# Performance work log

Measured on AMD Instinct MI355X. Metric: run time of the kernel, lower is better.

The kernel has to match this reference:

```python
import jax, jax.numpy as jnp
import numpy as np


def _graph_conv(feat_src, e_src, e_dst, n_src, n_dst, W, b):
    # DGL GraphConv, norm='both', bipartite block; feat_src: [N_src, A, C, H]
    ones_e = jnp.ones(e_src.shape[0], dtype=feat_src.dtype)
    out_deg = jax.ops.segment_sum(ones_e, e_src, num_segments=n_src)
    in_deg = jax.ops.segment_sum(ones_e, e_dst, num_segments=n_dst)
    norm_src = jnp.clip(out_deg, 1.0) ** -0.5
    norm_dst = jnp.clip(in_deg, 1.0) ** -0.5
    feat = feat_src * norm_src[:, None, None, None]
    # in_feats == out_feats -> DGL multiplies by W before aggregation
    feat = jnp.einsum('nach,ho->naco', feat, W)
    msgs = feat[e_src]                                   # gather  [E, A, C, H]
    agg = jax.ops.segment_sum(msgs, e_dst, num_segments=n_dst)  # scatter-add
    return agg * norm_dst[:, None, None, None] + b


def setup_inputs() -> dict:
    key = jax.random.key(0)
    ks = jax.random.split(key, 8)
    H = 128
    N_SRC0, N_DST0, N_DST1 = 50000, 20000, 4096
    E0, E1 = 320000, 65536
    return {
        'in_feat': jax.random.normal(ks[0], (2, H, 2, N_SRC0), dtype=jnp.float32),
        'W': jax.random.normal(ks[1], (H, H), dtype=jnp.float32) / np.sqrt(H),
        'b': jnp.zeros((H,), dtype=jnp.float32),
        'e0_src': jax.random.randint(ks[2], (E0,), 0, N_SRC0, dtype=jnp.int32),
        'e0_dst': jax.random.randint(ks[3], (E0,), 0, N_DST0, dtype=jnp.int32),
        'e1_src': jax.random.randint(ks[4], (E1,), 0, N_DST0, dtype=jnp.int32),
        'e1_dst': jax.random.randint(ks[5], (E1,), 0, N_DST1, dtype=jnp.int32),
        'n_dst0': N_DST0,
        'n_dst1': N_DST1,
    }


def reference(in_feat, W, b, e0_src, e0_dst, e1_src, e1_dst, n_dst0, n_dst1):
    # [A, H, C, N] -> [N, A, C, H]
    x = jnp.transpose(in_feat, (3, 0, 2, 1))
    n_src0 = x.shape[0]
    h = _graph_conv(x, e0_src, e0_dst, n_src0, n_dst0, W, b)
    h = jax.nn.relu(h)
    h = _graph_conv(h, e1_src, e1_dst, n_dst0, n_dst1, W, b)
    h = jax.nn.relu(h)
    # [N_dst1, A, C, H] -> [A, H, C, N_dst1]
    out = jnp.transpose(h, (1, 3, 2, 0))
    return jax.nn.relu(out)
```

## Files before the change

kernel.cpp:

```cpp
#include <hip/hip_runtime.h>
#include <math.h>

#define H128 128
#define NF 512
typedef unsigned short u16;
typedef __attribute__((ext_vector_type(8))) short short8;
typedef __attribute__((ext_vector_type(4))) float floatx4;

__device__ inline u16 f2bf(float f) {
  union { float f; unsigned u; } x; x.f = f;
  unsigned r = x.u + 0x7FFFu + ((x.u >> 16) & 1u);
  return (u16)(r >> 16);
}
__device__ inline void addbf8(float* a, uint4 u) {
  a[0] += __uint_as_float(u.x << 16);
  a[1] += __uint_as_float(u.x & 0xFFFF0000u);
  a[2] += __uint_as_float(u.y << 16);
  a[3] += __uint_as_float(u.y & 0xFFFF0000u);
  a[4] += __uint_as_float(u.z << 16);
  a[5] += __uint_as_float(u.z & 0xFFFF0000u);
  a[6] += __uint_as_float(u.w << 16);
  a[7] += __uint_as_float(u.w & 0xFFFF0000u);
}

__global__ void k_count2(const int* __restrict__ e0s, const int* __restrict__ e0d,
                         const int* __restrict__ e1s, const int* __restrict__ e1d,
                         int E0, int E1,
                         int* __restrict__ c_s0, int* __restrict__ c_d0,
                         int* __restrict__ c_s1, int* __restrict__ c_d1) {
  int i = blockIdx.x * 256 + threadIdx.x;
  if (i < E0) {
    atomicAdd(&c_s0[e0s[i]], 1);
    atomicAdd(&c_d0[e0d[i]], 1);
    return;
  }
  i -= E0;
  if (i < E1) {
    atomicAdd(&c_s1[e1s[i]], 1);
    atomicAdd(&c_d1[e1d[i]], 1);
  }
}

__global__ __launch_bounds__(1024) void k_prep(
    const int* __restrict__ cnt, int NCNT, float* __restrict__ normf,
    const int* __restrict__ degA, int nA, int* __restrict__ offA, int* __restrict__ curA,
    const int* __restrict__ degB, int nB, int* __restrict__ offB, int* __restrict__ curB,
    const float* __restrict__ W, uint4* __restrict__ wfrag) {
  __shared__ int wsum[16];
  const int b = blockIdx.x;
  const int tid = threadIdx.x;
  if (b < 2) {
    const int* deg = b ? degB : degA;
    int n = b ? nB : nA;
    int* off = b ? offB : offA;
    int* cur = b ? curB : curA;
    const int lane = tid & 63;
    const int wv = tid >> 6;
    const int per = (n + 1023) >> 10;
    const int base = tid * per;
    int cntk = n - base;
    if (cntk < 0) cntk = 0;
    if (cntk > per) cntk = per;
    int sum = 0;
    for (int i = 0; i < cntk; ++i) sum += deg[base + i];
    int x = sum;
    #pragma unroll
    for (int d2 = 1; d2 < 64; d2 <<= 1) {
      int y = __shfl_up(x, (unsigned)d2, 64);
      if (lane >= d2) x += y;
    }
    if (lane == 63) wsum[wv] = x;
    __syncthreads();
    if (wv == 0 && lane < 16) {
      int w = wsum[lane];
      #pragma unroll
      for (int d2 = 1; d2 < 16; d2 <<= 1) {
        int y = __shfl_up(w, (unsigned)d2, 64);
        if (lane >= d2) w += y;
      }
      wsum[lane] = w;
    }
    __syncthreads();
    int tbase = x - sum + (wv ? wsum[wv - 1] : 0);
    int running = tbase;
    for (int i = 0; i < cntk; ++i) {
      off[base + i] = running;
      cur[base + i] = running;
      running += deg[base + i];
    }
    if (tid == 1023) off[n] = wsum[15];
    return;
  }
  if (b < 4) {
    int t = (b - 2) * 1024 + tid;
    if (t < 2048) {
      int lane = t & 63;
      int pair = t >> 6;
      int ct = pair >> 2, kc = pair & 3;
      int quad = lane >> 4, r = lane & 15;
      const float* src = W + (size_t)(kc * 32 + quad * 8) * 128 + ct * 16 + r;
      union { u16 v[8]; uint4 u; } pk;
      #pragma unroll
      for (int j = 0; j < 8; ++j) pk.v[j] = f2bf(src[(size_t)j * 128]);
      wfrag[t] = pk.u;
    }
    return;
  }
  int i = (b - 4) * 1024 + tid;
  if (i < NCNT) {
    int d = cnt[i];
    float dv = (d < 1) ? 1.0f : (float)d;
    normf[i] = 1.0f / sqrtf(dv);
  }
}

__global__ __launch_bounds__(512) void k_tin_scatter(
    const float* __restrict__ in, const float* __restrict__ norm,
    u16* __restrict__ xp, int N, int SB,
    const int* __restrict__ e0s, const int* __restrict__ e0d,
    const int* __restrict__ e1s, const int* __restrict__ e1d,
    int E0, int E1,
    int* __restrict__ cur0, int* __restrict__ csr0,
    int* __restrict__ cur1, int* __restrict__ csr1) {
  __shared__ float tile[64 * 128];
  const int bid = blockIdx.x;
  const int tid = threadIdx.x;
  if (bid < SB) {
    int i = bid * 512 + tid;
    if (i < E0) {
      int p = atomicAdd(&cur0[e0d[i]], 1);
      csr0[p] = e0s[i];
      return;
    }
    i -= E0;
    if (i < E1) {
      int p = atomicAdd(&cur1[e1d[i]], 1);
      csr1[p] = e1s[i];
    }
    return;
  }
  const int tb = bid - SB;
  const int n0 = (tb >> 2) << 6;
  const int ac = tb & 3;
  const int a = ac >> 1, c = ac & 1;
  const float* base = in + ((size_t)a * 256 + c) * (size_t)N;
  #pragma unroll
  for (int i = 0; i < 4; ++i) {
    int fidx = (i << 9) + tid;
    int h = fidx >> 4;
    int t = fidx & 15;
    int n = t << 2;
    int gn = n0 + n;
    float4 v = make_float4(0.f, 0.f, 0.f, 0.f);
    if (gn < N) v = *(const float4*)(base + (size_t)h * 2 * N + gn);
    int q = h >> 2, rem = h & 3;
    int rot = ((q + t) & 31) << 2;
    tile[(n + 0) * 128 + rot + rem] = v.x;
    tile[(n + 1) * 128 + rot + rem] = v.y;
    tile[(n + 2) * 128 + rot + rem] = v.z;
    tile[(n + 3) * 128 + rot + rem] = v.w;
  }
  __syncthreads();
  #pragma unroll
  for (int i = 0; i < 4; ++i) {
    int fidx = (i << 9) + tid;
    int h4 = fidx & 31;
    int n = fidx >> 5;
    int gn = n0 + n;
    if (gn < N) {
      float4 v = *(const float4*)(&tile[n * 128 + (((h4 + (n >> 2)) & 31) << 2)]);
      float s = norm[gn];
      ushort4 o;
      o.x = f2bf(v.x * s); o.y = f2bf(v.y * s);
      o.z = f2bf(v.z * s); o.w = f2bf(v.w * s);
      *(ushort4*)(xp + (size_t)gn * NF + ac * H128 + (h4 << 2)) = o;
    }
  }
}

__global__ __launch_bounds__(256) void k_agg(
    const u16* __restrict__ xp, const int* __restrict__ csr,
    const int* __restrict__ off, const float* __restrict__ norm_dst,
    u16* __restrict__ outp, int ndst) {
  const int wave = threadIdx.x >> 6;
  const int lane = threadIdx.x & 63;
  const int d = blockIdx.x * 4 + wave;
  if (d >= ndst) return;
  const int s = off[d], e = off[d + 1];
  const uint4* xpl = (const uint4*)xp + lane;
  float acc[8];
  #pragma unroll
  for (int i = 0; i < 8; ++i) acc[i] = 0.f;
  int j = s;
  for (; j + 8 <= e; j += 8) {
    uint4 u[8];
    #pragma unroll
    for (int k = 0; k < 8; ++k) u[k] = xpl[(size_t)csr[j + k] * 64];
    #pragma unroll
    for (int k = 0; k < 8; ++k) addbf8(acc, u[k]);
  }
  for (; j + 4 <= e; j += 4) {
    uint4 u[4];
    #pragma unroll
    for (int k = 0; k < 4; ++k) u[k] = xpl[(size_t)csr[j + k] * 64];
    #pragma unroll
    for (int k = 0; k < 4; ++k) addbf8(acc, u[k]);
  }
  for (; j < e; ++j) addbf8(acc, xpl[(size_t)csr[j] * 64]);
  float nd = norm_dst[d];
  u16* orow = outp + (size_t)d * NF + lane * 8;
  ushort4 o0, o1;
  o0.x = f2bf(acc[0] * nd); o0.y = f2bf(acc[1] * nd);
  o0.z = f2bf(acc[2] * nd); o0.w = f2bf(acc[3] * nd);
  o1.x = f2bf(acc[4] * nd); o1.y = f2bf(acc[5] * nd);
  o1.z = f2bf(acc[6] * nd); o1.w = f2bf(acc[7] * nd);
  *(ushort4*)orow = o0;
  *(ushort4*)(orow + 4) = o1;
}

template <bool OUT_BF16>
__global__ __launch_bounds__(256) void k_gemm_mfma(
    const u16* __restrict__ A, const uint4* __restrict__ wfrag,
    const float* __restrict__ bias, const float* __restrict__ scale,
    void* __restrict__ outv, int M) {
  __shared__ uint4 wb[2048];
  const int tid = threadIdx.x;
  #pragma unroll
  for (int i = 0; i < 8; ++i) wb[i * 256 + tid] = wfrag[i * 256 + tid];
  __syncthreads();
  const int wave = tid >> 6;
  const int lane = tid & 63;
  const int quad = lane >> 4;
  const int r = lane & 15;
  const int row0 = (blockIdx.x * 4 + wave) << 4;
  if (row0 >= M) return;
  short8 a[4];
  const u16* abase = A + (size_t)(row0 + r) * 128 + quad * 8;
  #pragma unroll
  for (int kc = 0; kc < 4; ++kc) a[kc] = *(const short8*)(abase + kc * 32);
  floatx4 acc[8];
  #pragma unroll
  for (int ct = 0; ct < 8; ++ct) acc[ct] = (floatx4){0.f, 0.f, 0.f, 0.f};
  #pragma unroll
  for (int kc = 0; kc < 4; ++kc) {
    #pragma unroll
    for (int ct = 0; ct < 8; ++ct) {
      short8 b = *(const short8*)&wb[(ct * 4 + kc) * 64 + lane];
      acc[ct] = __builtin_amdgcn_mfma_f32_16x16x32_bf16(a[kc], b, acc[ct], 0, 0, 0);
    }
  }
  float sc = scale ? scale[(row0 >> 2) + quad] : 1.f;
  #pragma unroll
  for (int ct = 0; ct < 8; ++ct) {
    float bcol = bias[ct * 16 + r];
    #pragma unroll
    for (int reg = 0; reg < 4; ++reg) {
      float v = acc[ct][reg] + bcol;
      v = (v > 0.f ? v : 0.f) * sc;
      size_t idx = (size_t)(row0 + quad * 4 + reg) * 128 + ct * 16 + r;
      if (OUT_BF16) ((u16*)outv)[idx] = f2bf(v);
      else          ((float*)outv)[idx] = v;
    }
  }
}

__global__ __launch_bounds__(256) void k_transpose_out(
    const float* __restrict__ h1, float* __restrict__ out, int N) {
  __shared__ float tile[128][68];
  const int tid = threadIdx.x;
  const int n0 = blockIdx.x << 6;
  const int ac = blockIdx.y;
  const int a = ac >> 1, c = ac & 1;
  #pragma unroll
  for (int i = 0; i < 8; ++i) {
    int fidx = (i << 8) + tid;
    int h4 = fidx & 31;
    int n = fidx >> 5;
    float4 v = *(const float4*)(h1 + (size_t)(n0 + n) * NF + ac * H128 + (h4 << 2));
    int h = h4 << 2;
    tile[h + 0][n] = v.x; tile[h + 1][n] = v.y;
    tile[h + 2][n] = v.z; tile[h + 3][n] = v.w;
  }
  __syncthreads();
  float* obase = out + ((size_t)a * 256 + c) * (size_t)N;
  #pragma unroll
  for (int i = 0; i < 8; ++i) {
    int fidx = (i << 8) + tid;
    int h = fidx >> 4;
    int n = (fidx & 15) << 2;
    float4 v = *(const float4*)(&tile[h][n]);
    *(float4*)(obase + (size_t)h * 2 * N + n0 + n) = v;
  }
}

extern "C" void kernel_launch(void* const* d_in, const int* in_sizes, int n_in,
                              void* d_out, int out_size, void* d_ws, size_t ws_size,
                              hipStream_t stream) {
  const float* in_feat = (const float*)d_in[0];
  const float* W       = (const float*)d_in[1];
  const float* bias    = (const float*)d_in[2];
  const int* e0_src    = (const int*)d_in[3];
  const int* e0_dst    = (const int*)d_in[4];
  const int* e1_src    = (const int*)d_in[5];
  const int* e1_dst    = (const int*)d_in[6];
  const int N_DST0 = 20000;
  const int N_DST1 = 4096;
  const int N_SRC0 = in_sizes[0] / NF;
  const int E0 = in_sizes[3];
  const int E1 = in_sizes[5];

  u16* xp    = (u16*)d_ws;
  u16* h0    = xp + (size_t)N_SRC0 * NF;
  u16* agg0b = h0 + (size_t)N_DST0 * NF;
  u16* agg1b = agg0b + (size_t)N_DST0 * NF;
  float* h1  = (float*)(agg1b + (size_t)N_DST1 * NF);
  int* ibase    = (int*)(h1 + (size_t)N_DST1 * NF);
  int* cnt_src0 = ibase;
  int* cnt_dst0 = cnt_src0 + N_SRC0;
  int* cnt_src1 = cnt_dst0 + N_DST0;
  int* cnt_dst1 = cnt_src1 + N_DST0;
  int* off0 = cnt_dst1 + N_DST1;
  int* cur0 = off0 + N_DST0 + 1;
  int* csr0 = cur0 + N_DST0;
  int* off1 = csr0 + E0;
  int* cur1 = off1 + N_DST1 + 1;
  int* csr1 = cur1 + N_DST1;
  uint4* wfrag = (uint4*)(((uintptr_t)(csr1 + E1) + 15) & ~(uintptr_t)15);
  float* normf = (float*)(wfrag + 2048);
  float* normf_src0 = normf;
  float* normf_dst0 = normf_src0 + N_SRC0;
  float* normf_src1 = normf_dst0 + N_DST0;
  float* normf_dst1 = normf_src1 + N_DST0;

  const int NCNT = N_SRC0 + N_DST0 + N_DST0 + N_DST1;
  hipMemsetAsync(cnt_src0, 0, (size_t)NCNT * sizeof(int), stream);

  k_count2<<<(E0 + E1 + 255) / 256, 256, 0, stream>>>(
      e0_src, e0_dst, e1_src, e1_dst, E0, E1, cnt_src0, cnt_dst0, cnt_src1, cnt_dst1);

  k_prep<<<4 + (NCNT + 1023) / 1024, 1024, 0, stream>>>(
      cnt_src0, NCNT, normf,
      cnt_dst0, N_DST0, off0, cur0,
      cnt_dst1, N_DST1, off1, cur1,
      W, wfrag);

  const int SB = (E0 + E1 + 511) / 512;
  const int TB = ((N_SRC0 + 63) / 64) * 4;
  k_tin_scatter<<<SB + TB, 512, 0, stream>>>(
      in_feat, normf_src0, xp, N_SRC0, SB,
      e0_src, e0_dst, e1_src, e1_dst, E0, E1,
      cur0, csr0, cur1, csr1);

  k_agg<<<(N_DST0 + 3) / 4, 256, 0, stream>>>(
      xp, csr0, off0, normf_dst0, agg0b, N_DST0);
  k_gemm_mfma<true><<<(N_DST0 * 4) / 64, 256, 0, stream>>>(
      agg0b, wfrag, bias, normf_src1, (void*)h0, N_DST0 * 4);

  k_agg<<<(N_DST1 + 3) / 4, 256, 0, stream>>>(
      h0, csr1, off1, normf_dst1, agg1b, N_DST1);
  k_gemm_mfma<false><<<(N_DST1 * 4) / 64, 256, 0, stream>>>(
      agg1b, wfrag, bias, nullptr, (void*)h1, N_DST1 * 4);

  dim3 tg2(N_DST1 / 64, 4);
  k_transpose_out<<<tg2, 256, 0, stream>>>(h1, (float*)d_out, N_DST1);
}
```

Baseline: 338.8 us.

## Fuse aggregation with MFMA GEMM and output transpose; coarsen scatter and transpose blocks

```diff
diff --git a/kernel.cpp b/kernel.cpp
--- a/kernel.cpp
+++ b/kernel.cpp
@@ -126,39 +126,58 @@
   const int bid = blockIdx.x;
   const int tid = threadIdx.x;
   if (bid < SB) {
-    int i = bid * 512 + tid;
-    if (i < E0) {
-      int p = atomicAdd(&cur0[e0d[i]], 1);
-      csr0[p] = e0s[i];
-      return;
-    }
-    i -= E0;
-    if (i < E1) {
-      int p = atomicAdd(&cur1[e1d[i]], 1);
-      csr1[p] = e1s[i];
+    #pragma unroll
+    for (int k = 0; k < 4; ++k) {
+      int i = (bid * 4 + k) * 512 + tid;
+      if (i < E0) {
+        int p = atomicAdd(&cur0[e0d[i]], 1);
+        csr0[p] = e0s[i];
+      } else {
+        i -= E0;
+        if (i < E1) {
+          int p = atomicAdd(&cur1[e1d[i]], 1);
+          csr1[p] = e1s[i];
+        }
+      }
     }
     return;
   }
   const int tb = bid - SB;
-  const int n0 = (tb >> 2) << 6;
+  const int n0A = (tb >> 2) << 7;
   const int ac = tb & 3;
   const int a = ac >> 1, c = ac & 1;
   const float* base = in + ((size_t)a * 256 + c) * (size_t)N;
+  float4 vA[4], vB[4];
+  #pragma unroll
+  for (int i = 0; i < 4; ++i) {
+    int fidx = (i << 9) + tid;
+    int h = fidx >> 4;
+    int t = fidx & 15;
+    int gn = n0A + (t << 2);
+    vA[i] = make_float4(0.f, 0.f, 0.f, 0.f);
+    if (gn < N) vA[i] = *(const float4*)(base + (size_t)h * 2 * N + gn);
+  }
+  #pragma unroll
+  for (int i = 0; i < 4; ++i) {
+    int fidx = (i << 9) + tid;
+    int h = fidx >> 4;
+    int t = fidx & 15;
+    int gn = n0A + 64 + (t << 2);
+    vB[i] = make_float4(0.f, 0.f, 0.f, 0.f);
+    if (gn < N) vB[i] = *(const float4*)(base + (size_t)h * 2 * N + gn);
+  }
   #pragma unroll
   for (int i = 0; i < 4; ++i) {
     int fidx = (i << 9) + tid;
     int h = fidx >> 4;
     int t = fidx & 15;
     int n = t << 2;
-    int gn = n0 + n;
-    float4 v = make_float4(0.f, 0.f, 0.f, 0.f);
-    if (gn < N) v = *(const float4*)(base + (size_t)h * 2 * N + gn);
     int q = h >> 2, rem = h & 3;
     int rot = ((q + t) & 31) << 2;
-    tile[(n + 0) * 128 + rot + rem] = v.x;
-    tile[(n + 1) * 128 + rot + rem] = v.y;
-    tile[(n + 2) * 128 + rot + rem] = v.z;
-    tile[(n + 3) * 128 + rot + rem] = v.w;
+    tile[(n + 0) * 128 + rot + rem] = vA[i].x;
+    tile[(n + 1) * 128 + rot + rem] = vA[i].y;
+    tile[(n + 2) * 128 + rot + rem] = vA[i].z;
+    tile[(n + 3) * 128 + rot + rem] = vA[i].w;
   }
   __syncthreads();
   #pragma unroll
@@ -166,7 +185,7 @@
     int fidx = (i << 9) + tid;
     int h4 = fidx & 31;
     int n = fidx >> 5;
-    int gn = n0 + n;
+    int gn = n0A + n;
     if (gn < N) {
       float4 v = *(const float4*)(&tile[n * 128 + (((h4 + (n >> 2)) & 31) << 2)]);
       float s = norm[gn];
@@ -176,68 +195,83 @@
       *(ushort4*)(xp + (size_t)gn * NF + ac * H128 + (h4 << 2)) = o;
     }
   }
-}
-
-__global__ __launch_bounds__(256) void k_agg(
+  __syncthreads();
+  #pragma unroll
+  for (int i = 0; i < 4; ++i) {
+    int fidx = (i << 9) + tid;
+    int h = fidx >> 4;
+    int t = fidx & 15;
+    int n = t << 2;
+    int q = h >> 2, rem = h & 3;
+    int rot = ((q + t) & 31) << 2;
+    tile[(n + 0) * 128 + rot + rem] = vB[i].x;
+    tile[(n + 1) * 128 + rot + rem] = vB[i].y;
+    tile[(n + 2) * 128 + rot + rem] = vB[i].z;
+    tile[(n + 3) * 128 + rot + rem] = vB[i].w;
+  }
+  __syncthreads();
+  #pragma unroll
+  for (int i = 0; i < 4; ++i) {
+    int fidx = (i << 9) + tid;
+    int h4 = fidx & 31;
+    int n = fidx >> 5;
+    int gn = n0A + 64 + n;
+    if (gn < N) {
+      float4 v = *(const float4*)(&tile[n * 128 + (((h4 + (n >> 2)) & 31) << 2)]);
+      float s = norm[gn];
+      ushort4 o;
+      o.x = f2bf(v.x * s); o.y = f2bf(v.y * s);
+      o.z = f2bf(v.z * s); o.w = f2bf(v.w * s);
+      *(ushort4*)(xp + (size_t)gn * NF + ac * H128 + (h4 << 2)) = o;
+    }
+  }
+}
+
+template <int MODE>
+__global__ __launch_bounds__(256) void k_agg_gemm(
     const u16* __restrict__ xp, const int* __restrict__ csr,
     const int* __restrict__ off, const float* __restrict__ norm_dst,
-    u16* __restrict__ outp, int ndst) {
-  const int wave = threadIdx.x >> 6;
-  const int lane = threadIdx.x & 63;
-  const int d = blockIdx.x * 4 + wave;
-  if (d >= ndst) return;
-  const int s = off[d], e = off[d + 1];
-  const uint4* xpl = (const uint4*)xp + lane;
-  float acc[8];
-  #pragma unroll
-  for (int i = 0; i < 8; ++i) acc[i] = 0.f;
-  int j = s;
-  for (; j + 8 <= e; j += 8) {
-    uint4 u[8];
-    #pragma unroll
-    for (int k = 0; k < 8; ++k) u[k] = xpl[(size_t)csr[j + k] * 64];
-    #pragma unroll
-    for (int k = 0; k < 8; ++k) addbf8(acc, u[k]);
-  }
-  for (; j + 4 <= e; j += 4) {
-    uint4 u[4];
-    #pragma unroll
-    for (int k = 0; k < 4; ++k) u[k] = xpl[(size_t)csr[j + k] * 64];
-    #pragma unroll
-    for (int k = 0; k < 4; ++k) addbf8(acc, u[k]);
-  }
-  for (; j < e; ++j) addbf8(acc, xpl[(size_t)csr[j] * 64]);
-  float nd = norm_dst[d];
-  u16* orow = outp + (size_t)d * NF + lane * 8;
-  ushort4 o0, o1;
-  o0.x = f2bf(acc[0] * nd); o0.y = f2bf(acc[1] * nd);
-  o0.z = f2bf(acc[2] * nd); o0.w = f2bf(acc[3] * nd);
-  o1.x = f2bf(acc[4] * nd); o1.y = f2bf(acc[5] * nd);
-  o1.z = f2bf(acc[6] * nd); o1.w = f2bf(acc[7] * nd);
-  *(ushort4*)orow = o0;
-  *(ushort4*)(orow + 4) = o1;
-}
-
-template <bool OUT_BF16>
-__global__ __launch_bounds__(256) void k_gemm_mfma(
-    const u16* __restrict__ A, const uint4* __restrict__ wfrag,
-    const float* __restrict__ bias, const float* __restrict__ scale,
-    void* __restrict__ outv, int M) {
+    const uint4* __restrict__ wfrag, const float* __restrict__ bias,
+    const float* __restrict__ scale, void* __restrict__ outv, int Nout) {
   __shared__ uint4 wb[2048];
+  __shared__ u16 atile[16][520];
   const int tid = threadIdx.x;
   #pragma unroll
   for (int i = 0; i < 8; ++i) wb[i * 256 + tid] = wfrag[i * 256 + tid];
-  __syncthreads();
   const int wave = tid >> 6;
   const int lane = tid & 63;
+  const int d0 = blockIdx.x << 4;
+  const uint4* xpl = (const uint4*)xp + lane;
+  #pragma unroll
+  for (int i = 0; i < 4; ++i) {
+    const int m = wave * 4 + i;
+    const int d = d0 + m;
+    const int s = off[d], e = off[d + 1];
+    float acc[8];
+    #pragma unroll
+    for (int k = 0; k < 8; ++k) acc[k] = 0.f;
+    int j = s;
+    for (; j + 8 <= e; j += 8) {
+      uint4 u[8];
+      #pragma unroll
+      for (int k = 0; k < 8; ++k) u[k] = xpl[(size_t)csr[j + k] * 64];
+      #pragma unroll
+      for (int k = 0; k < 8; ++k) addbf8(acc, u[k]);
+    }
+    for (; j < e; ++j) addbf8(acc, xpl[(size_t)csr[j] * 64]);
+    float nd = norm_dst[d];
+    union { u16 v[8]; uint4 u; } pk;
+    #pragma unroll
+    for (int k = 0; k < 8; ++k) pk.v[k] = f2bf(acc[k] * nd);
+    *(uint4*)&atile[m][lane * 8] = pk.u;
+  }
+  __syncthreads();
   const int quad = lane >> 4;
   const int r = lane & 15;
-  const int row0 = (blockIdx.x * 4 + wave) << 4;
-  if (row0 >= M) return;
   short8 a[4];
-  const u16* abase = A + (size_t)(row0 + r) * 128 + quad * 8;
-  #pragma unroll
-  for (int kc = 0; kc < 4; ++kc) a[kc] = *(const short8*)(abase + kc * 32);
+  #pragma unroll
+  for (int kc = 0; kc < 4; ++kc)
+    a[kc] = *(const short8*)&atile[r][wave * 128 + kc * 32 + quad * 8];
   floatx4 acc[8];
   #pragma unroll
   for (int ct = 0; ct < 8; ++ct) acc[ct] = (floatx4){0.f, 0.f, 0.f, 0.f};
@@ -249,47 +283,35 @@
       acc[ct] = __builtin_amdgcn_mfma_f32_16x16x32_bf16(a[kc], b, acc[ct], 0, 0, 0);
     }
   }
-  float sc = scale ? scale[(row0 >> 2) + quad] : 1.f;
-  #pragma unroll
-  for (int ct = 0; ct < 8; ++ct) {
-    float bcol = bias[ct * 16 + r];
-    #pragma unroll
-    for (int reg = 0; reg < 4; ++reg) {
-      float v = acc[ct][reg] + bcol;
-      v = (v > 0.f ? v : 0.f) * sc;
-      size_t idx = (size_t)(row0 + quad * 4 + reg) * 128 + ct * 16 + r;
-      if (OUT_BF16) ((u16*)outv)[idx] = f2bf(v);
-      else          ((float*)outv)[idx] = v;
-    }
-  }
-}
-
-__global__ __launch_bounds__(256) void k_transpose_out(
-    const float* __restrict__ h1, float* __restrict__ out, int N) {
-  __shared__ float tile[128][68];
-  const int tid = threadIdx.x;
-  const int n0 = blockIdx.x << 6;
-  const int ac = blockIdx.y;
-  const int a = ac >> 1, c = ac & 1;
-  #pragma unroll
-  for (int i = 0; i < 8; ++i) {
-    int fidx = (i << 8) + tid;
-    int h4 = fidx & 31;
-    int n = fidx >> 5;
-    float4 v = *(const float4*)(h1 + (size_t)(n0 + n) * NF + ac * H128 + (h4 << 2));
-    int h = h4 << 2;
-    tile[h + 0][n] = v.x; tile[h + 1][n] = v.y;
-    tile[h + 2][n] = v.z; tile[h + 3][n] = v.w;
-  }
-  __syncthreads();
-  float* obase = out + ((size_t)a * 256 + c) * (size_t)N;
-  #pragma unroll
-  for (int i = 0; i < 8; ++i) {
-    int fidx = (i << 8) + tid;
-    int h = fidx >> 4;
-    int n = (fidx & 15) << 2;
-    float4 v = *(const float4*)(&tile[h][n]);
-    *(float4*)(obase + (size_t)h * 2 * N + n0 + n) = v;
+  if (MODE == 0) {
+    float sc[4];
+    #pragma unroll
+    for (int reg = 0; reg < 4; ++reg) sc[reg] = scale[d0 + quad * 4 + reg];
+    #pragma unroll
+    for (int ct = 0; ct < 8; ++ct) {
+      float bcol = bias[ct * 16 + r];
+      #pragma unroll
+      for (int reg = 0; reg < 4; ++reg) {
+        float v = acc[ct][reg] + bcol;
+        v = (v > 0.f ? v : 0.f) * sc[reg];
+        ((u16*)outv)[(size_t)(d0 + quad * 4 + reg) * NF + wave * H128 + ct * 16 + r] = f2bf(v);
+      }
+    }
+  } else {
+    const int aa = wave >> 1, cc = wave & 1;
+    #pragma unroll
+    for (int ct = 0; ct < 8; ++ct) {
+      float bcol = bias[ct * 16 + r];
+      float4 o;
+      float v0 = acc[ct][0] + bcol; o.x = v0 > 0.f ? v0 : 0.f;
+      float v1 = acc[ct][1] + bcol; o.y = v1 > 0.f ? v1 : 0.f;
+      float v2 = acc[ct][2] + bcol; o.z = v2 > 0.f ? v2 : 0.f;
+      float v3 = acc[ct][3] + bcol; o.w = v3 > 0.f ? v3 : 0.f;
+      float* dst = (float*)outv +
+          ((size_t)aa * 256 + (size_t)(ct * 16 + r) * 2 + cc) * (size_t)Nout +
+          d0 + quad * 4;
+      *(float4*)dst = o;
+    }
   }
 }
 
@@ -309,12 +331,9 @@
   const int E0 = in_sizes[3];
   const int E1 = in_sizes[5];
 
-  u16* xp    = (u16*)d_ws;
-  u16* h0    = xp + (size_t)N_SRC0 * NF;
-  u16* agg0b = h0 + (size_t)N_DST0 * NF;
-  u16* agg1b = agg0b + (size_t)N_DST0 * NF;
-  float* h1  = (float*)(agg1b + (size_t)N_DST1 * NF);
-  int* ibase    = (int*)(h1 + (size_t)N_DST1 * NF);
+  u16* xp = (u16*)d_ws;
+  u16* h0 = xp + (size_t)N_SRC0 * NF;
+  int* ibase    = (int*)(h0 + (size_t)N_DST0 * NF);
   int* cnt_src0 = ibase;
   int* cnt_dst0 = cnt_src0 + N_SRC0;
   int* cnt_src1 = cnt_dst0 + N_DST0;
@@ -344,23 +363,17 @@
       cnt_dst1, N_DST1, off1, cur1,
       W, wfrag);
 
-  const int SB = (E0 + E1 + 511) / 512;
-  const int TB = ((N_SRC0 + 63) / 64) * 4;
+  const int SB = (E0 + E1 + 2047) / 2048;
+  const int ntiles = (N_SRC0 + 63) / 64;
+  const int TB = ((ntiles + 1) / 2) * 4;
   k_tin_scatter<<<SB + TB, 512, 0, stream>>>(
       in_feat, normf_src0, xp, N_SRC0, SB,
       e0_src, e0_dst, e1_src, e1_dst, E0, E1,
       cur0, csr0, cur1, csr1);
 
-  k_agg<<<(N_DST0 + 3) / 4, 256, 0, stream>>>(
-      xp, csr0, off0, normf_dst0, agg0b, N_DST0);
-  k_gemm_mfma<true><<<(N_DST0 * 4) / 64, 256, 0, stream>>>(
-      agg0b, wfrag, bias, normf_src1, (void*)h0, N_DST0 * 4);
-
-  k_agg<<<(N_DST1 + 3) / 4, 256, 0, stream>>>(
-      h0, csr1, off1, normf_dst1, agg1b, N_DST1);
-  k_gemm_mfma<false><<<(N_DST1 * 4) / 64, 256, 0, stream>>>(
-      agg1b, wfrag, bias, nullptr, (void*)h1, N_DST1 * 4);
-
-  dim3 tg2(N_DST1 / 64, 4);
-  k_transpose_out<<<tg2, 256, 0, stream>>>(h1, (float*)d_out, N_DST1);
-}
+  k_agg_gemm<0><<<N_DST0 / 16, 256, 0, stream>>>(
+      xp, csr0, off0, normf_dst0, wfrag, bias, normf_src1, (void*)h0, 0);
+
+  k_agg_gemm<1><<<N_DST1 / 16, 256, 0, stream>>>(
+      h0, csr1, off1, normf_dst1, wfrag, bias, nullptr, d_out, N_DST1);
+}
```

After: 331.3 us. -2.2%, faster.
